# Kernel tuning notes

Hardware: AMD Instinct MI355X
Metric: run time of the kernel (lower is better)

The kernel has to match this reference:

```python
import jax, jax.numpy as jnp
import numpy as np

B, L, HID = 2, 4096, 2048
H, D = 16, HID // 16          # num_heads, head_dim = 128
C = 64                        # chunk_size
LOWR = 16                     # gate low-rank dim
GLN = 16.0                    # gate_logit_normalizer
EPS = 1e-5


def setup_inputs() -> dict:
    key = jax.random.key(0)
    ks = jax.random.split(key, 10)
    s = lambda fan_in: 1.0 / np.sqrt(fan_in)
    return {
        "x": jax.random.normal(ks[0], (B, L, HID), jnp.float32),
        "Wq": jax.random.normal(ks[1], (HID, HID), jnp.float32) * s(HID),
        "Wk": jax.random.normal(ks[2], (HID, HID), jnp.float32) * s(HID),
        "Wv": jax.random.normal(ks[3], (HID, HID), jnp.float32) * s(HID),
        "Wg1": jax.random.normal(ks[4], (HID, LOWR), jnp.float32) * s(HID),
        "Wg2": jax.random.normal(ks[5], (LOWR, HID), jnp.float32) * s(LOWR),
        "bg2": jax.random.normal(ks[6], (HID,), jnp.float32) * 0.1,
        "Wgate": jax.random.normal(ks[7], (HID, HID), jnp.float32) * s(HID),
        "norm_w": jnp.ones((D,), jnp.float32),
        "Wo": jax.random.normal(ks[8], (HID, HID), jnp.float32) * s(HID),
    }


def _gla_forward(x, Wq, Wk, Wv, Wg1, Wg2, bg2, Wgate, norm_w, Wo):
    Bx, Lx, _ = x.shape
    NC = Lx // C
    scale = D ** (-0.5)

    def heads(y):  # [B,L,HID] -> [B,H,L,D]
        return y.reshape(Bx, Lx, H, D).transpose(0, 2, 1, 3)

    q = heads(x @ Wq)
    k = heads(x @ Wk)
    v = heads(x @ Wv)
    gk = heads(jax.nn.log_sigmoid((x @ Wg1) @ Wg2 + bg2) / GLN)

    # chunked layout [NC,B,H,C,D]; cumulative log-gates within each chunk
    def chunked(y):
        return y.reshape(Bx, H, NC, C, D).transpose(2, 0, 1, 3, 4)

    qc, kc, vc = chunked(q), chunked(k), chunked(v)
    Gc = jnp.cumsum(chunked(gk), axis=3)

    tril = jnp.tril(jnp.ones((C, C), bool))
    S0 = jnp.zeros((Bx, H, D, D), jnp.float32)

    def step(S, inp):
        Q, K, V, G = inp                       # [B,H,C,D]
        Gbase = G[:, :, 0]                     # [B,H,D] cumsum at chunk start
        # inter-chunk: decayed query against carried state
        qg = Q * scale * jnp.exp(G)
        o_inter = jnp.einsum('bhld,bhdv->bhlv', qg, S)
        # intra-chunk causal attention with relative decay
        Qh = Q * jnp.exp(G - Gbase[:, :, None]) * scale
        Kh = K * jnp.exp(Gbase[:, :, None] - G)
        A = jnp.einsum('bhld,bhsd->bhls', Qh, Kh)
        A = jnp.where(tril, A, 0.0)
        o_intra = jnp.einsum('bhls,bhsv->bhlv', A, V)
        # state update
        glast = G[:, :, -1]                    # [B,H,D]
        Ks = K * jnp.exp(glast[:, :, None] - G)
        S_new = S * jnp.exp(glast)[..., None] + jnp.einsum('bhld,bhlv->bhdv', Ks, V)
        return S_new, o_inter + o_intra

    S_final, o_chunks = jax.lax.scan(step, S0, (qc, kc, vc, Gc))
    # [NC,B,H,C,D] -> [B,L,H,D]
    o = o_chunks.transpose(1, 3, 0, 2, 4).reshape(Bx, Lx, H, D)  # wrong order guard below
    o = o_chunks.transpose(1, 2, 0, 3, 4).reshape(Bx, H, Lx, D).transpose(0, 2, 1, 3)

    # RMSNorm over head_dim
    o = o * jax.lax.rsqrt(jnp.mean(o * o, axis=-1, keepdims=True) + EPS) * norm_w
    o = o.reshape(Bx, Lx, HID)

    g = x @ Wgate
    o = o * (g * jax.nn.sigmoid(g))            # swish output gate
    return o @ Wo, S_final


def reference(x, Wq, Wk, Wv, Wg1, Wg2, bg2, Wgate, norm_w, Wo):
    return _gla_forward(x, Wq, Wk, Wv, Wg1, Wg2, bg2, Wgate, norm_w, Wo)
```

## Files before the change

### kernel.cpp

```cpp
#include <hip/hip_runtime.h>
#include <math.h>

typedef __bf16 bf16;
typedef __attribute__((ext_vector_type(8))) __bf16 bf16x8;
typedef __attribute__((ext_vector_type(4))) __bf16 bf16x4;
typedef __attribute__((ext_vector_type(4))) float f32x4;

#define AS1 __attribute__((address_space(1)))
#define AS3 __attribute__((address_space(3)))

__device__ __forceinline__ void async16(const void* g, void* l) {
  __builtin_amdgcn_global_load_lds((AS1 void*)g, (AS3 void*)l, 16, 0, 0);
}

__device__ __forceinline__ f32x4 mfma16(bf16x8 a, bf16x8 b, f32x4 c) {
  return __builtin_amdgcn_mfma_f32_16x16x32_bf16(a, b, c, 0, 0, 0);
}

__device__ __forceinline__ float logsig(float z) {
  return fminf(z, 0.f) - __logf(1.f + __expf(-fabsf(z)));
}

static constexpr float SCALE = 0.088388347648318447f;


__global__ __launch_bounds__(256) void transpose_w(const float* __restrict__ W, bf16* __restrict__ Wt) {
  __shared__ float tl[64][65];
  int n0 = blockIdx.x * 64, k0 = blockIdx.y * 64;
  for (int e = threadIdx.x; e < 4096; e += 256) {
    int i = e >> 6, j = e & 63;
    tl[i][j] = W[(size_t)(k0 + i) * 2048 + n0 + j];
  }
  __syncthreads();
  for (int e = threadIdx.x; e < 4096; e += 256) {
    int i = e >> 6, j = e & 63;
    Wt[(size_t)(n0 + i) * 2048 + k0 + j] = (bf16)tl[j][i];
  }
}

__global__ __launch_bounds__(256) void cvt_x(const float* __restrict__ x, bf16* __restrict__ xb, int n) {
  for (size_t i = ((size_t)blockIdx.x * 256 + threadIdx.x) * 4; i < (size_t)n; i += (size_t)gridDim.x * 1024) {
    f32x4 v = *(const f32x4*)&x[i];
    bf16x4 o;
    #pragma unroll
    for (int j = 0; j < 4; ++j) o[j] = (bf16)v[j];
    *(bf16x4*)&xb[i] = o;
  }
}

__global__ __launch_bounds__(256) void cvt_wg1(const float* __restrict__ Wg1, bf16* __restrict__ Wg1t) {
  int k = blockIdx.x * 256 + threadIdx.x;
  #pragma unroll
  for (int j = 0; j < 16; ++j) Wg1t[j * 2048 + k] = (bf16)Wg1[(size_t)k * 16 + j];
}

__global__ __launch_bounds__(256) void xg_mfma(const bf16* __restrict__ xb, const bf16* __restrict__ Wg1t,
                                               float* __restrict__ xg) {
  int wave = threadIdx.x >> 6, lane = threadIdx.x & 63;
  int row0 = blockIdx.x * 64 + wave * 16;
  int rsel = lane & 15, klo = (lane >> 4) * 8;
  f32x4 acc = {0.f, 0.f, 0.f, 0.f};
  #pragma unroll 4
  for (int kt = 0; kt < 2048; kt += 32) {
    bf16x8 a = *(const bf16x8*)&xb[(size_t)(row0 + rsel) * 2048 + kt + klo];
    bf16x8 b = *(const bf16x8*)&Wg1t[rsel * 2048 + kt + klo];
    acc = mfma16(a, b, acc);
  }
  int col = lane & 15, r0 = (lane >> 4) * 4;
  #pragma unroll
  for (int r = 0; r < 4; ++r) xg[(size_t)(row0 + r0 + r) * 16 + col] = acc[r];
}


__device__ __forceinline__ int swzi(int r, int k0) { return r * 64 + ((((k0 >> 3) ^ r) & 7) << 3) + (k0 & 7); }

__device__ __forceinline__ void stage_half(const bf16* __restrict__ Gp, bf16* lds, int rbase, int kt, int h,
                                           int Kdim, int wave, int lane) {
  #pragma unroll
  for (int ii = 0; ii < 2; ++ii) {
    int i = 2 * h + ii;
    int row = (i * 8 + wave) * 8 + (lane >> 3);
    int gcol = (lane & 7) ^ ((lane >> 3) & 7);
    async16(&Gp[(size_t)(rbase + row) * Kdim + kt + gcol * 8], lds + (i * 8 + wave) * 512);
  }
}

template <int OUTF32>
__global__ __launch_bounds__(512, 2) void gemm256(const bf16* __restrict__ A, const bf16* __restrict__ Bt,
                                                  void* __restrict__ Cout, int Mdim, int Ndim, int Kdim) {
  __shared__ __align__(16) bf16 sA[2][256 * 64];
  __shared__ __align__(16) bf16 sB[2][256 * 64];

  int tid = threadIdx.x;
  int wave = tid >> 6, lane = tid & 63;
  int wr = wave >> 2, wc = wave & 3;
  int rsel = lane & 15, klo = (lane >> 4) * 8;

  int nwg = gridDim.x;
  int cpx = nwg >> 3;
  int bid = blockIdx.x;
  int swzb = (bid & 7) * cpx + (bid >> 3);
  int nbx = Ndim >> 8;
  int mt = (swzb / nbx) << 8, nt = (swzb % nbx) << 8;

  const int NT = Kdim >> 6;

  stage_half(A, &sA[0][0], mt, 0, 0, Kdim, wave, lane);
  stage_half(A, &sA[0][0], mt, 0, 1, Kdim, wave, lane);
  stage_half(Bt, &sB[0][0], nt, 0, 0, Kdim, wave, lane);
  stage_half(Bt, &sB[0][0], nt, 0, 1, Kdim, wave, lane);
  if (NT > 1) {
    stage_half(A, &sA[1][0], mt, 64, 0, Kdim, wave, lane);
    stage_half(A, &sA[1][0], mt, 64, 1, Kdim, wave, lane);
    stage_half(Bt, &sB[1][0], nt, 64, 0, Kdim, wave, lane);
    stage_half(Bt, &sB[1][0], nt, 64, 1, Kdim, wave, lane);
    asm volatile("s_waitcnt vmcnt(8)" ::: "memory");
  } else {
    asm volatile("s_waitcnt vmcnt(0)" ::: "memory");
  }
  __builtin_amdgcn_sched_barrier(0);
  __builtin_amdgcn_s_barrier();

  f32x4 z4 = {0.f, 0.f, 0.f, 0.f};
  f32x4 acc[8][4];
  #pragma unroll
  for (int i = 0; i < 8; ++i)
    #pragma unroll
    for (int j = 0; j < 4; ++j) acc[i][j] = z4;

  bf16x8 bfr[4][2];

  for (int t = 0; t < NT; ++t) {
    int b = t & 1;
    const bf16* __restrict__ cA = &sA[b][0];
    const bf16* __restrict__ cB = &sB[b][0];
    #pragma unroll
    for (int q = 0; q < 4; ++q) {
      bf16x8 af[2][2];
      if (q == 0) {
        #pragma unroll
        for (int nf = 0; nf < 4; ++nf)
          #pragma unroll
          for (int ks = 0; ks < 2; ++ks)
            bfr[nf][ks] = *(const bf16x8*)&cB[swzi(wc * 64 + nf * 16 + rsel, ks * 32 + klo)];
      }
      #pragma unroll
      for (int i = 0; i < 2; ++i)
        #pragma unroll
        for (int ks = 0; ks < 2; ++ks)
          af[i][ks] = *(const bf16x8*)&cA[swzi(wr * 128 + (2 * q + i) * 16 + rsel, ks * 32 + klo)];

      if (q < 2) {
        if (t >= 1 && t + 1 < NT) stage_half(A, &sA[(t + 1) & 1][0], mt, (t + 1) * 64, q, Kdim, wave, lane);
      } else {
        if (t + 2 < NT) stage_half(Bt, &sB[b][0], nt, (t + 2) * 64, q - 2, Kdim, wave, lane);
      }

      if (q == 3) {
        if (t + 2 < NT) {
          asm volatile("s_waitcnt vmcnt(4)" ::: "memory");
        } else if (t + 1 < NT) {
          asm volatile("s_waitcnt vmcnt(0)" ::: "memory");
        }
        __builtin_amdgcn_sched_barrier(0);
      }

      __builtin_amdgcn_s_barrier();
      asm volatile("s_waitcnt lgkmcnt(0)" ::: "memory");
      __builtin_amdgcn_sched_barrier(0);
      __builtin_amdgcn_s_setprio(1);
      #pragma unroll
      for (int i = 0; i < 2; ++i)
        #pragma unroll
        for (int nf = 0; nf < 4; ++nf)
          #pragma unroll
          for (int ks = 0; ks < 2; ++ks)
            acc[2 * q + i][nf] = mfma16(af[i][ks], bfr[nf][ks], acc[2 * q + i][nf]);
      __builtin_amdgcn_s_setprio(0);
      __builtin_amdgcn_s_barrier();
    }
  }

  int col0 = nt + wc * 64 + (lane & 15);
  int row0 = mt + wr * 128 + (lane >> 4) * 4;
  for (int mf = 0; mf < 8; ++mf)
    for (int nf = 0; nf < 4; ++nf)
      #pragma unroll
      for (int r = 0; r < 4; ++r) {
        size_t idx = (size_t)(row0 + mf * 16 + r) * Ndim + col0 + nf * 16;
        if constexpr (OUTF32 != 0)
          ((float*)Cout)[idx] = acc[mf][nf][r];
        else
          ((bf16*)Cout)[idx] = (bf16)acc[mf][nf][r];
      }
}


__global__ __launch_bounds__(256, 3) void gate_stage(bf16* __restrict__ qb, bf16* __restrict__ kb,
                                                     const float* __restrict__ xg, const float* __restrict__ Wg2,
                                                     const float* __restrict__ bg2, float* __restrict__ adec,
                                                     float* __restrict__ eg0) {
  __shared__ float G[64][132];
  __shared__ float xgs[1024];
  __shared__ float wg2s[2048];
  __shared__ float bg2s[128];
  int bid = blockIdx.x;
  int c = bid & 63, bh = bid >> 6, h = bh & 15;
  int l0row = (bh >> 4) * 4096 + c * 64;
  int tid = threadIdx.x;

  for (int e = tid; e < 1024; e += 256) xgs[e] = xg[(size_t)(l0row + (e >> 4)) * 16 + (e & 15)];
  for (int e = tid; e < 2048; e += 256) wg2s[e] = Wg2[(size_t)(e >> 7) * 2048 + h * 128 + (e & 127)];
  if (tid < 128) bg2s[tid] = bg2[h * 128 + tid];
  __syncthreads();

  {
    int d = tid & 127, half = tid >> 7;
    float w[16];
    #pragma unroll
    for (int j = 0; j < 16; ++j) w[j] = wg2s[j * 128 + d];
    float bz = bg2s[d];
    float run = 0.f;
    #pragma unroll 4
    for (int l = 0; l < 32; ++l) {
      int lr = half * 32 + l;
      float z = bz;
      #pragma unroll
      for (int j = 0; j < 16; ++j) z += xgs[lr * 16 + j] * w[j];
      run += logsig(z) * (1.0f / 16.0f);
      G[lr][d] = run;
    }
  }
  __syncthreads();
  {
    int d = tid & 127, half = tid >> 7;
    if (half) {
      float base = G[31][d];
      #pragma unroll 4
      for (int l = 32; l < 64; ++l) G[l][d] += base;
    }
  }
  __syncthreads();

  for (int it = 0; it < 4; ++it) {
    int l = (tid >> 4) + it * 16;
    int d0 = (tid & 15) * 8;
    size_t ro = (size_t)(l0row + l) * 2048 + h * 128 + d0;
    bf16x8 qv = *(const bf16x8*)&qb[ro];
    bf16x8 kv = *(const bf16x8*)&kb[ro];
    bf16x8 qo, ko;
    #pragma unroll
    for (int i = 0; i < 8; ++i) {
      int d = d0 + i;
      float Gl = G[l][d], Gb = G[0][d];
      qo[i] = (bf16)((float)qv[i] * SCALE * __expf(Gl - Gb));
      ko[i] = (bf16)((float)kv[i] * __expf(Gb - Gl));
    }
    *(bf16x8*)&qb[ro] = qo;
    *(bf16x8*)&kb[ro] = ko;
  }
  if (tid < 128) {
    float g63 = G[63][tid], g0 = G[0][tid];
    adec[(size_t)bid * 128 + tid] = __expf(g63);
    eg0[(size_t)bid * 128 + tid] = __expf(g0);
  }
}


__global__ __launch_bounds__(256, 4) void phaseA(const bf16* __restrict__ kh, const bf16* __restrict__ vb,
                                                 const float* __restrict__ adec, const float* __restrict__ eg0,
                                                 bf16* __restrict__ U) {
  __shared__ __align__(16) bf16 KhT[128][76];
  __shared__ __align__(16) bf16 VT[128][76];
  __shared__ float cscs[128];
  int bid = blockIdx.x;
  int c = bid & 63, bh = bid >> 6, h = bh & 15;
  int l0row = (bh >> 4) * 4096 + c * 64;
  int tid = threadIdx.x;
  if (tid < 128) cscs[tid] = adec[(size_t)bid * 128 + tid] / eg0[(size_t)bid * 128 + tid];

  for (int it = 0; it < 4; ++it) {
    int l = (tid >> 4) + it * 16;
    int d0 = (tid & 15) * 8;
    size_t ro = (size_t)(l0row + l) * 2048 + h * 128 + d0;
    bf16x8 kv = *(const bf16x8*)&kh[ro];
    bf16x8 vv = *(const bf16x8*)&vb[ro];
    #pragma unroll
    for (int i = 0; i < 8; ++i) {
      KhT[d0 + i][l] = kv[i];
      VT[d0 + i][l] = vv[i];
    }
  }
  __syncthreads();

  int wave = tid >> 6, lane = tid & 63;
  int rsel = lane & 15, klo = (lane >> 4) * 8;
  f32x4 z4 = {0.f, 0.f, 0.f, 0.f};
  f32x4 acc[2][8];
  for (int i = 0; i < 2; ++i)
    for (int j = 0; j < 8; ++j) acc[i][j] = z4;
  #pragma unroll
  for (int ks = 0; ks < 2; ++ks) {
    bf16x8 a0 = *(const bf16x8*)&VT[(wave * 2 + 0) * 16 + rsel][ks * 32 + klo];
    bf16x8 a1 = *(const bf16x8*)&VT[(wave * 2 + 1) * 16 + rsel][ks * 32 + klo];
    #pragma unroll
    for (int j = 0; j < 8; ++j) {
      bf16x8 bb = *(const bf16x8*)&KhT[j * 16 + rsel][ks * 32 + klo];
      acc[0][j] = mfma16(a0, bb, acc[0][j]);
      acc[1][j] = mfma16(a1, bb, acc[1][j]);
    }
  }
  size_t ub = (size_t)bid * 16384;
  for (int i = 0; i < 2; ++i)
    for (int j = 0; j < 8; ++j)
      #pragma unroll
      for (int r = 0; r < 4; ++r) {
        int vr = (wave * 2 + i) * 16 + (lane >> 4) * 4 + r;
        int d = j * 16 + (lane & 15);
        U[ub + (size_t)vr * 128 + d] = (bf16)(acc[i][j][r] * cscs[d]);
      }
}


__global__ __launch_bounds__(256) void phaseB(bf16* __restrict__ U, const float* __restrict__ adec,
                                              float* __restrict__ Sfin) {
  int bh = blockIdx.x >> 4, vg = blockIdx.x & 15;
  int t = threadIdx.x;
  int v = vg * 8 + (t >> 5);
  int d0 = (t & 31) * 4;
  float S[4] = {0.f, 0.f, 0.f, 0.f};
  size_t base = (size_t)bh * 64 * 16384 + (size_t)v * 128 + d0;
  size_t abase = (size_t)bh * 64 * 128 + d0;
  bf16x4 u = *(const bf16x4*)&U[base];
  f32x4 a = *(const f32x4*)&adec[abase];
  for (int c = 0; c < 64; ++c) {
    bf16x4 un = u;
    f32x4 an = a;
    if (c < 63) {
      un = *(const bf16x4*)&U[base + (size_t)(c + 1) * 16384];
      an = *(const f32x4*)&adec[abase + (size_t)(c + 1) * 128];
    }
    bf16x4 sv;
    #pragma unroll
    for (int i = 0; i < 4; ++i) sv[i] = (bf16)S[i];
    *(bf16x4*)&U[base + (size_t)c * 16384] = sv;
    #pragma unroll
    for (int i = 0; i < 4; ++i) S[i] = S[i] * a[i] + (float)u[i];
    u = un;
    a = an;
  }
  #pragma unroll
  for (int i = 0; i < 4; ++i) Sfin[((size_t)bh * 128 + d0 + i) * 128 + v] = S[i];
}


__global__ __launch_bounds__(256, 3) void phaseC(const bf16* __restrict__ qh, const bf16* __restrict__ kh,
                                                 const bf16* __restrict__ vb, const bf16* __restrict__ Sc,
                                                 const float* __restrict__ eg0, const bf16* __restrict__ gb,
                                                 const float* __restrict__ nw, bf16* __restrict__ ob) {
  __shared__ __align__(16) char lds[48384];
  bf16(*Qh)[136] = (bf16(*)[136])(lds);
  bf16(*VT)[76] = (bf16(*)[76])(lds + 17408);
  bf16(*A_lds)[76] = (bf16(*)[76])(lds + 36864);
  float* eG0s = (float*)(lds + 46592);
  float* red = (float*)(lds + 47104);
  float* rsq = (float*)(lds + 48128);
  float(*o_lds)[132] = (float(*)[132])(lds);

  int bid = blockIdx.x;
  int c = bid & 63, bh = bid >> 6, h = bh & 15;
  int l0row = (bh >> 4) * 4096 + c * 64;
  int tid = threadIdx.x;

  for (int it = 0; it < 4; ++it) {
    int e = tid + it * 256;
    int l = e >> 4, d0 = (e & 15) * 8;
    *(bf16x8*)&Qh[l][d0] = *(const bf16x8*)&qh[(size_t)(l0row + l) * 2048 + h * 128 + d0];
  }
  for (int it = 0; it < 4; ++it) {
    int l = (tid >> 4) + it * 16;
    int d0 = (tid & 15) * 8;
    bf16x8 vv = *(const bf16x8*)&vb[(size_t)(l0row + l) * 2048 + h * 128 + d0];
    #pragma unroll
    for (int i = 0; i < 8; ++i) VT[d0 + i][l] = vv[i];
  }
  if (tid < 128) eG0s[tid] = eg0[(size_t)bid * 128 + tid];
  __syncthreads();

  int wave = tid >> 6, lane = tid & 63;
  int rsel = lane & 15, klo = (lane >> 4) * 8;
  f32x4 z4 = {0.f, 0.f, 0.f, 0.f};

  bf16x8 bbk[4];
  #pragma unroll
  for (int ks = 0; ks < 4; ++ks)
    bbk[ks] = *(const bf16x8*)&kh[(size_t)(l0row + wave * 16 + rsel) * 2048 + h * 128 + ks * 32 + klo];
  bf16x8 scr[4][2];
  #pragma unroll
  for (int ks = 0; ks < 4; ++ks)
    #pragma unroll
    for (int j = 0; j < 2; ++j)
      scr[ks][j] =
          *(const bf16x8*)&Sc[(size_t)bid * 16384 + (size_t)((wave * 2 + j) * 16 + rsel) * 128 + ks * 32 + klo];

  f32x4 accA[4];
  for (int i = 0; i < 4; ++i) accA[i] = z4;
  #pragma unroll
  for (int ks = 0; ks < 4; ++ks)
    #pragma unroll
    for (int mf = 0; mf < 4; ++mf) {
      bf16x8 aa = *(const bf16x8*)&Qh[mf * 16 + rsel][ks * 32 + klo];
      accA[mf] = mfma16(aa, bbk[ks], accA[mf]);
    }
  #pragma unroll
  for (int mf = 0; mf < 4; ++mf)
    #pragma unroll
    for (int r = 0; r < 4; ++r) {
      int lrow = mf * 16 + (lane >> 4) * 4 + r;
      int scol = wave * 16 + (lane & 15);
      A_lds[lrow][scol] = (bf16)(scol <= lrow ? accA[mf][r] : 0.0f);
    }

  bf16x8 bs[4][2];
  #pragma unroll
  for (int ks = 0; ks < 4; ++ks)
    #pragma unroll
    for (int j = 0; j < 2; ++j)
      #pragma unroll
      for (int i = 0; i < 8; ++i) bs[ks][j][i] = (bf16)((float)scr[ks][j][i] * eG0s[ks * 32 + klo + i]);

  f32x4 accO[4][2];
  for (int i = 0; i < 4; ++i)
    for (int j = 0; j < 2; ++j) accO[i][j] = z4;
  #pragma unroll
  for (int ks = 0; ks < 4; ++ks)
    #pragma unroll
    for (int mf = 0; mf < 4; ++mf) {
      bf16x8 aa = *(const bf16x8*)&Qh[mf * 16 + rsel][ks * 32 + klo];
      accO[mf][0] = mfma16(aa, bs[ks][0], accO[mf][0]);
      accO[mf][1] = mfma16(aa, bs[ks][1], accO[mf][1]);
    }
  __syncthreads();

  #pragma unroll
  for (int ks = 0; ks < 2; ++ks) {
    bf16x8 b0 = *(const bf16x8*)&VT[(wave * 2 + 0) * 16 + rsel][ks * 32 + klo];
    bf16x8 b1 = *(const bf16x8*)&VT[(wave * 2 + 1) * 16 + rsel][ks * 32 + klo];
    #pragma unroll
    for (int mf = 0; mf < 4; ++mf) {
      bf16x8 aa = *(const bf16x8*)&A_lds[mf * 16 + rsel][ks * 32 + klo];
      accO[mf][0] = mfma16(aa, b0, accO[mf][0]);
      accO[mf][1] = mfma16(aa, b1, accO[mf][1]);
    }
  }
  __syncthreads();

  #pragma unroll
  for (int mf = 0; mf < 4; ++mf)
    #pragma unroll
    for (int j = 0; j < 2; ++j)
      #pragma unroll
      for (int r = 0; r < 4; ++r)
        o_lds[mf * 16 + (lane >> 4) * 4 + r][(wave * 2 + j) * 16 + (lane & 15)] = accO[mf][j][r];
  __syncthreads();

  {
    int row = tid >> 2, part = tid & 3;
    float ss = 0.f;
    #pragma unroll
    for (int i = 0; i < 32; ++i) {
      float xv = o_lds[row][part * 32 + i];
      ss += xv * xv;
    }
    red[row * 4 + part] = ss;
  }
  __syncthreads();
  if (tid < 64) {
    float s = red[tid * 4] + red[tid * 4 + 1] + red[tid * 4 + 2] + red[tid * 4 + 3];
    rsq[tid] = rsqrtf(s * (1.0f / 128.0f) + 1e-5f);
  }
  __syncthreads();
  for (int e = tid; e < 8192; e += 256) {
    int l = e >> 7, d = e & 127;
    float ov = o_lds[l][d] * rsq[l] * nw[d];
    float gf = (float)gb[(size_t)(l0row + l) * 2048 + h * 128 + d];
    float sil = gf / (1.0f + __expf(-gf));
    ob[(size_t)(l0row + l) * 2048 + h * 128 + d] = (bf16)(ov * sil);
  }
}


extern "C" void kernel_launch(void* const* d_in, const int* in_sizes, int n_in, void* d_out, int out_size,
                              void* d_ws, size_t ws_size, hipStream_t stream) {
  const float* x = (const float*)d_in[0];
  const float* Wq = (const float*)d_in[1];
  const float* Wk = (const float*)d_in[2];
  const float* Wv = (const float*)d_in[3];
  const float* Wg1 = (const float*)d_in[4];
  const float* Wg2 = (const float*)d_in[5];
  const float* bg2 = (const float*)d_in[6];
  const float* Wgate = (const float*)d_in[7];
  const float* nw = (const float*)d_in[8];
  const float* Wo = (const float*)d_in[9];
  float* out1 = (float*)d_out;
  float* out2 = out1 + (size_t)8192 * 2048;

  const size_t WT_B = (size_t)2048 * 2048 * 2;
  const size_t XG_B = (size_t)8192 * 16 * 4;
  const size_t WG1_B = (size_t)16 * 2048 * 2;
  const size_t TOK_B = (size_t)8192 * 2048 * 2;
  const size_t VEC_B = (size_t)2048 * 128 * 4;
  const size_t U_B = (size_t)32 * 64 * 16384 * 2;

  char* ws = (char*)d_ws;
  bf16* Wt = (bf16*)ws;
  float* xgf = (float*)(ws + WT_B);
  bf16* Wg1t = (bf16*)(ws + WT_B + XG_B);
  bf16* qb = (bf16*)(ws + WT_B + XG_B + WG1_B);
  bf16* kbuf = (bf16*)(ws + WT_B + XG_B + WG1_B + TOK_B);
  bf16* vbuf = (bf16*)(ws + WT_B + XG_B + WG1_B + 2 * TOK_B);
  bf16* gbuf = (bf16*)(ws + WT_B + XG_B + WG1_B + 3 * TOK_B);
  float* adecf = (float*)(ws + WT_B + XG_B + WG1_B + 4 * TOK_B);
  float* eg0f = (float*)(ws + WT_B + XG_B + WG1_B + 4 * TOK_B + VEC_B);
  bf16* Ub = (bf16*)(ws + WT_B + XG_B + WG1_B + 4 * TOK_B + 2 * VEC_B);
  bf16* xb = Ub;
  const size_t NEED = WT_B + XG_B + WG1_B + 4 * TOK_B + 2 * VEC_B + U_B;
  if (ws_size < NEED) return;

  dim3 tg(32, 32);

  cvt_x<<<4096, 256, 0, stream>>>(x, xb, 8192 * 2048);
  cvt_wg1<<<8, 256, 0, stream>>>(Wg1, Wg1t);
  xg_mfma<<<128, 256, 0, stream>>>(xb, Wg1t, xgf);

  transpose_w<<<tg, 256, 0, stream>>>(Wq, Wt);
  gemm256<0><<<256, 512, 0, stream>>>(xb, Wt, qb, 8192, 2048, 2048);
  transpose_w<<<tg, 256, 0, stream>>>(Wk, Wt);
  gemm256<0><<<256, 512, 0, stream>>>(xb, Wt, kbuf, 8192, 2048, 2048);
  transpose_w<<<tg, 256, 0, stream>>>(Wv, Wt);
  gemm256<0><<<256, 512, 0, stream>>>(xb, Wt, vbuf, 8192, 2048, 2048);
  transpose_w<<<tg, 256, 0, stream>>>(Wgate, Wt);
  gemm256<0><<<256, 512, 0, stream>>>(xb, Wt, gbuf, 8192, 2048, 2048);

  gate_stage<<<2048, 256, 0, stream>>>(qb, kbuf, xgf, Wg2, bg2, adecf, eg0f);
  phaseA<<<2048, 256, 0, stream>>>(kbuf, vbuf, adecf, eg0f, Ub);
  phaseB<<<512, 256, 0, stream>>>(Ub, adecf, out2);
  phaseC<<<2048, 256, 0, stream>>>(qb, kbuf, vbuf, Ub, eg0f, gbuf, nw, qb);

  transpose_w<<<tg, 256, 0, stream>>>(Wo, Wt);
  gemm256<1><<<256, 512, 0, stream>>>(qb, Wt, out1, 8192, 2048, 2048);
}
```

Measured before the change: 601.8 us.

## Restructure GEMM main loop with register double-buffered fragments and one barrier per tile

Rewrites the 256x256 bf16 GEMM inner loop. LDS fragment reads now ping-pong between two register sets so the next A/B fragments load while the current MFMA phase runs. The per-quarter s_barrier/lgkmcnt pairs become a single barrier per K-tile, and the first fragments of the next tile are read ahead of the last MFMA phase. In exchange, global prefetch drops from two tiles ahead to one with a full vmcnt(0) wait each tile, which may expose memory latency. LDS reads issued just before the barrier are not explicitly waited on, leaving a subtle buffer-reuse ordering risk.

```diff
diff --git a/kernel.cpp b/kernel.cpp
--- a/kernel.cpp
+++ b/kernel.cpp
@@ -85,6 +85,20 @@
   }
 }
 
+__device__ __forceinline__ void mfma_phase(f32x4 (&acc)[8][4], int row0, const bf16x8 (&AF)[2][2],
+                                           const bf16x8 (&B0)[4], const bf16x8 (&B1)[4]) {
+  __builtin_amdgcn_sched_barrier(0);
+  __builtin_amdgcn_s_setprio(1);
+  #pragma unroll
+  for (int ks = 0; ks < 2; ++ks)
+    #pragma unroll
+    for (int i = 0; i < 2; ++i)
+      #pragma unroll
+      for (int nf = 0; nf < 4; ++nf)
+        acc[row0 + i][nf] = mfma16(AF[i][ks], ks ? B1[nf] : B0[nf], acc[row0 + i][nf]);
+  __builtin_amdgcn_s_setprio(0);
+}
+
 template <int OUTF32>
 __global__ __launch_bounds__(512, 2) void gemm256(const bf16* __restrict__ A, const bf16* __restrict__ Bt,
                                                   void* __restrict__ Cout, int Mdim, int Ndim, int Kdim) {
@@ -105,21 +119,27 @@
 
   const int NT = Kdim >> 6;
 
+  auto rdA = [&](bf16x8 (&dst)[2][2], const bf16* base, int m0) {
+    #pragma unroll
+    for (int i = 0; i < 2; ++i)
+      #pragma unroll
+      for (int ks = 0; ks < 2; ++ks)
+        dst[i][ks] = *(const bf16x8*)&base[swzi(wr * 128 + (m0 + i) * 16 + rsel, ks * 32 + klo)];
+  };
+  auto rdB = [&](bf16x8 (&dst)[4], const bf16* base, int ks) {
+    #pragma unroll
+    for (int nf = 0; nf < 4; ++nf)
+      dst[nf] = *(const bf16x8*)&base[swzi(wc * 64 + nf * 16 + rsel, ks * 32 + klo)];
+  };
+
   stage_half(A, &sA[0][0], mt, 0, 0, Kdim, wave, lane);
   stage_half(A, &sA[0][0], mt, 0, 1, Kdim, wave, lane);
   stage_half(Bt, &sB[0][0], nt, 0, 0, Kdim, wave, lane);
   stage_half(Bt, &sB[0][0], nt, 0, 1, Kdim, wave, lane);
-  if (NT > 1) {
-    stage_half(A, &sA[1][0], mt, 64, 0, Kdim, wave, lane);
-    stage_half(A, &sA[1][0], mt, 64, 1, Kdim, wave, lane);
-    stage_half(Bt, &sB[1][0], nt, 64, 0, Kdim, wave, lane);
-    stage_half(Bt, &sB[1][0], nt, 64, 1, Kdim, wave, lane);
-    asm volatile("s_waitcnt vmcnt(8)" ::: "memory");
-  } else {
-    asm volatile("s_waitcnt vmcnt(0)" ::: "memory");
-  }
+  asm volatile("s_waitcnt vmcnt(0)" ::: "memory");
   __builtin_amdgcn_sched_barrier(0);
   __builtin_amdgcn_s_barrier();
+  __builtin_amdgcn_sched_barrier(0);
 
   f32x4 z4 = {0.f, 0.f, 0.f, 0.f};
   f32x4 acc[8][4];
@@ -128,57 +148,58 @@
     #pragma unroll
     for (int j = 0; j < 4; ++j) acc[i][j] = z4;
 
-  bf16x8 bfr[4][2];
+  bf16x8 aP[2][2], aQ[2][2], b0[4], b1[4];
+  rdB(b0, &sB[0][0], 0);
+  rdA(aP, &sA[0][0], 0);
 
   for (int t = 0; t < NT; ++t) {
-    int b = t & 1;
-    const bf16* __restrict__ cA = &sA[b][0];
-    const bf16* __restrict__ cB = &sB[b][0];
-    #pragma unroll
-    for (int q = 0; q < 4; ++q) {
-      bf16x8 af[2][2];
-      if (q == 0) {
-        #pragma unroll
-        for (int nf = 0; nf < 4; ++nf)
-          #pragma unroll
-          for (int ks = 0; ks < 2; ++ks)
-            bfr[nf][ks] = *(const bf16x8*)&cB[swzi(wc * 64 + nf * 16 + rsel, ks * 32 + klo)];
-      }
-      #pragma unroll
-      for (int i = 0; i < 2; ++i)
-        #pragma unroll
-        for (int ks = 0; ks < 2; ++ks)
-          af[i][ks] = *(const bf16x8*)&cA[swzi(wr * 128 + (2 * q + i) * 16 + rsel, ks * 32 + klo)];
-
-      if (q < 2) {
-        if (t >= 1 && t + 1 < NT) stage_half(A, &sA[(t + 1) & 1][0], mt, (t + 1) * 64, q, Kdim, wave, lane);
-      } else {
-        if (t + 2 < NT) stage_half(Bt, &sB[b][0], nt, (t + 2) * 64, q - 2, Kdim, wave, lane);
-      }
-
-      if (q == 3) {
-        if (t + 2 < NT) {
-          asm volatile("s_waitcnt vmcnt(4)" ::: "memory");
-        } else if (t + 1 < NT) {
-          asm volatile("s_waitcnt vmcnt(0)" ::: "memory");
-        }
-        __builtin_amdgcn_sched_barrier(0);
-      }
-
+    const bf16* cA = &sA[t & 1][0];
+    const bf16* cB = &sB[t & 1][0];
+    bf16* nAp = &sA[(t & 1) ^ 1][0];
+    bf16* nBp = &sB[(t & 1) ^ 1][0];
+    bool more = (t + 1) < NT;
+
+    if (more) {
+      stage_half(A, nAp, mt, (t + 1) * 64, 0, Kdim, wave, lane);
+      stage_half(A, nAp, mt, (t + 1) * 64, 1, Kdim, wave, lane);
+    }
+    rdB(b1, cB, 1);
+    rdA(aQ, cA, 2);
+    mfma_phase(acc, 0, aP, b0, b1);
+
+    if (more) {
+      stage_half(Bt, nBp, nt, (t + 1) * 64, 0, Kdim, wave, lane);
+      stage_half(Bt, nBp, nt, (t + 1) * 64, 1, Kdim, wave, lane);
+    }
+    rdA(aP, cA, 4);
+    mfma_phase(acc, 2, aQ, b0, b1);
+
+    rdA(aQ, cA, 6);
+    mfma_phase(acc, 4, aP, b0, b1);
+    if (more) {
+      asm volatile("s_waitcnt vmcnt(0)" ::: "memory");
+      __builtin_amdgcn_sched_barrier(0);
       __builtin_amdgcn_s_barrier();
-      asm volatile("s_waitcnt lgkmcnt(0)" ::: "memory");
       __builtin_amdgcn_sched_barrier(0);
-      __builtin_amdgcn_s_setprio(1);
-      #pragma unroll
-      for (int i = 0; i < 2; ++i)
-        #pragma unroll
-        for (int nf = 0; nf < 4; ++nf)
-          #pragma unroll
-          for (int ks = 0; ks < 2; ++ks)
-            acc[2 * q + i][nf] = mfma16(af[i][ks], bfr[nf][ks], acc[2 * q + i][nf]);
-      __builtin_amdgcn_s_setprio(0);
-      __builtin_amdgcn_s_barrier();
-    }
+    }
+
+    __builtin_amdgcn_s_setprio(1);
+    #pragma unroll
+    for (int i = 0; i < 2; ++i)
+      #pragma unroll
+      for (int nf = 0; nf < 4; ++nf) acc[6 + i][nf] = mfma16(aQ[i][0], b0[nf], acc[6 + i][nf]);
+    __builtin_amdgcn_s_setprio(0);
+    if (more) {
+      rdB(b0, nBp, 0);
+      rdA(aP, nAp, 0);
+    }
+    __builtin_amdgcn_sched_barrier(0);
+    __builtin_amdgcn_s_setprio(1);
+    #pragma unroll
+    for (int i = 0; i < 2; ++i)
+      #pragma unroll
+      for (int nf = 0; nf < 4; ++nf) acc[6 + i][nf] = mfma16(aQ[i][1], b1[nf], acc[6 + i][nf]);
+    __builtin_amdgcn_s_setprio(0);
   }
 
   int col0 = nt + wc * 64 + (lane & 15);
```

Result: faster. 565.9 us (-6.0%).

## Fuse Q/K/V/gate projections into one GEMM and deepen LDS pipeline

Applied to the files above, without the earlier changes.

The four projection GEMMs become a single 8192x8192x2048 launch over concatenated transposed weights. The output is scattered into the separate q/k/v/g buffers through a group stride. The GEMM main loop now stages K-tiles of 32 into a 4-deep LDS ring buffer with register double-buffering of fragments, so prefetch overlaps MFMA work. The intent is to cut launch overhead and tail effects and to hide global load latency better, at the cost of more complex wait accounting and reuse of the U workspace region for the weights.

```diff
diff --git a/kernel.cpp b/kernel.cpp
--- a/kernel.cpp
+++ b/kernel.cpp
@@ -72,24 +72,28 @@
 }
 
 
-__device__ __forceinline__ int swzi(int r, int k0) { return r * 64 + ((((k0 >> 3) ^ r) & 7) << 3) + (k0 & 7); }
-
-__device__ __forceinline__ void stage_half(const bf16* __restrict__ Gp, bf16* lds, int rbase, int kt, int h,
-                                           int Kdim, int wave, int lane) {
-  #pragma unroll
-  for (int ii = 0; ii < 2; ++ii) {
-    int i = 2 * h + ii;
-    int row = (i * 8 + wave) * 8 + (lane >> 3);
-    int gcol = (lane & 7) ^ ((lane >> 3) & 7);
-    async16(&Gp[(size_t)(rbase + row) * Kdim + kt + gcol * 8], lds + (i * 8 + wave) * 512);
+__device__ __forceinline__ int swz32(int r, int k0) {
+  int g = ((k0 >> 3) ^ (r & 3) ^ ((r >> 2) & 3)) & 3;
+  return r * 32 + g * 8 + (k0 & 7);
+}
+
+__device__ __forceinline__ void stage32(const bf16* __restrict__ Gp, bf16* lds, int rbase, int kt, int Kdim,
+                                        int tid) {
+  #pragma unroll
+  for (int i = 0; i < 2; ++i) {
+    int slot = i * 512 + tid;
+    int row = slot >> 2, gr = slot & 3;
+    int gsrc = (gr ^ (row & 3) ^ ((row >> 2) & 3)) & 3;
+    async16(&Gp[(size_t)(rbase + row) * Kdim + kt + gsrc * 8], lds + slot * 8);
   }
 }
 
 template <int OUTF32>
 __global__ __launch_bounds__(512, 2) void gemm256(const bf16* __restrict__ A, const bf16* __restrict__ Bt,
-                                                  void* __restrict__ Cout, int Mdim, int Ndim, int Kdim) {
-  __shared__ __align__(16) bf16 sA[2][256 * 64];
-  __shared__ __align__(16) bf16 sB[2][256 * 64];
+                                                  void* __restrict__ Cout, int Mdim, int Ndim, int Kdim,
+                                                  size_t groupStride) {
+  __shared__ __align__(16) bf16 sA[4][256 * 32];
+  __shared__ __align__(16) bf16 sB[4][256 * 32];
 
   int tid = threadIdx.x;
   int wave = tid >> 6, lane = tid & 63;
@@ -103,23 +107,29 @@
   int nbx = Ndim >> 8;
   int mt = (swzb / nbx) << 8, nt = (swzb % nbx) << 8;
 
-  const int NT = Kdim >> 6;
-
-  stage_half(A, &sA[0][0], mt, 0, 0, Kdim, wave, lane);
-  stage_half(A, &sA[0][0], mt, 0, 1, Kdim, wave, lane);
-  stage_half(Bt, &sB[0][0], nt, 0, 0, Kdim, wave, lane);
-  stage_half(Bt, &sB[0][0], nt, 0, 1, Kdim, wave, lane);
-  if (NT > 1) {
-    stage_half(A, &sA[1][0], mt, 64, 0, Kdim, wave, lane);
-    stage_half(A, &sA[1][0], mt, 64, 1, Kdim, wave, lane);
-    stage_half(Bt, &sB[1][0], nt, 64, 0, Kdim, wave, lane);
-    stage_half(Bt, &sB[1][0], nt, 64, 1, Kdim, wave, lane);
-    asm volatile("s_waitcnt vmcnt(8)" ::: "memory");
-  } else {
-    asm volatile("s_waitcnt vmcnt(0)" ::: "memory");
-  }
+  const int NT = Kdim >> 5;
+
+  auto rdA4 = [&](bf16x8 (&dst)[4], const bf16* base, int m0) {
+    #pragma unroll
+    for (int i = 0; i < 4; ++i)
+      dst[i] = *(const bf16x8*)&base[swz32(wr * 128 + (m0 + i) * 16 + rsel, klo)];
+  };
+  auto rdB4 = [&](bf16x8 (&dst)[4], const bf16* base) {
+    #pragma unroll
+    for (int nf = 0; nf < 4; ++nf)
+      dst[nf] = *(const bf16x8*)&base[swz32(wc * 64 + nf * 16 + rsel, klo)];
+  };
+
+  stage32(A, &sA[0][0], mt, 0, Kdim, tid);
+  stage32(Bt, &sB[0][0], nt, 0, Kdim, tid);
+  stage32(A, &sA[1][0], mt, 32, Kdim, tid);
+  stage32(Bt, &sB[1][0], nt, 32, Kdim, tid);
+  stage32(A, &sA[2][0], mt, 64, Kdim, tid);
+  stage32(Bt, &sB[2][0], nt, 64, Kdim, tid);
+  asm volatile("s_waitcnt vmcnt(8)" ::: "memory");
   __builtin_amdgcn_sched_barrier(0);
   __builtin_amdgcn_s_barrier();
+  __builtin_amdgcn_sched_barrier(0);
 
   f32x4 z4 = {0.f, 0.f, 0.f, 0.f};
   f32x4 acc[8][4];
@@ -128,66 +138,64 @@
     #pragma unroll
     for (int j = 0; j < 4; ++j) acc[i][j] = z4;
 
-  bf16x8 bfr[4][2];
+  bf16x8 aP[4], aQ[4], bC[4], aPn[4], bN[4];
+  rdB4(bC, &sB[0][0]);
+  rdA4(aP, &sA[0][0], 0);
 
   for (int t = 0; t < NT; ++t) {
-    int b = t & 1;
-    const bf16* __restrict__ cA = &sA[b][0];
-    const bf16* __restrict__ cB = &sB[b][0];
-    #pragma unroll
-    for (int q = 0; q < 4; ++q) {
-      bf16x8 af[2][2];
-      if (q == 0) {
-        #pragma unroll
-        for (int nf = 0; nf < 4; ++nf)
-          #pragma unroll
-          for (int ks = 0; ks < 2; ++ks)
-            bfr[nf][ks] = *(const bf16x8*)&cB[swzi(wc * 64 + nf * 16 + rsel, ks * 32 + klo)];
-      }
-      #pragma unroll
-      for (int i = 0; i < 2; ++i)
-        #pragma unroll
-        for (int ks = 0; ks < 2; ++ks)
-          af[i][ks] = *(const bf16x8*)&cA[swzi(wr * 128 + (2 * q + i) * 16 + rsel, ks * 32 + klo)];
-
-      if (q < 2) {
-        if (t >= 1 && t + 1 < NT) stage_half(A, &sA[(t + 1) & 1][0], mt, (t + 1) * 64, q, Kdim, wave, lane);
-      } else {
-        if (t + 2 < NT) stage_half(Bt, &sB[b][0], nt, (t + 2) * 64, q - 2, Kdim, wave, lane);
-      }
-
-      if (q == 3) {
-        if (t + 2 < NT) {
-          asm volatile("s_waitcnt vmcnt(4)" ::: "memory");
-        } else if (t + 1 < NT) {
-          asm volatile("s_waitcnt vmcnt(0)" ::: "memory");
-        }
-        __builtin_amdgcn_sched_barrier(0);
-      }
-
-      __builtin_amdgcn_s_barrier();
-      asm volatile("s_waitcnt lgkmcnt(0)" ::: "memory");
-      __builtin_amdgcn_sched_barrier(0);
-      __builtin_amdgcn_s_setprio(1);
-      #pragma unroll
-      for (int i = 0; i < 2; ++i)
-        #pragma unroll
-        for (int nf = 0; nf < 4; ++nf)
-          #pragma unroll
-          for (int ks = 0; ks < 2; ++ks)
-            acc[2 * q + i][nf] = mfma16(af[i][ks], bfr[nf][ks], acc[2 * q + i][nf]);
-      __builtin_amdgcn_s_setprio(0);
-      __builtin_amdgcn_s_barrier();
-    }
-  }
-
-  int col0 = nt + wc * 64 + (lane & 15);
+    const bf16* cA = &sA[t & 3][0];
+    const bf16* cB = &sB[t & 3][0];
+
+    if (t + 3 < NT) {
+      stage32(A, &sA[(t + 3) & 3][0], mt, (t + 3) * 32, Kdim, tid);
+      stage32(Bt, &sB[(t + 3) & 3][0], nt, (t + 3) * 32, Kdim, tid);
+    }
+    rdA4(aQ, cA, 4);
+    __builtin_amdgcn_sched_barrier(0);
+    __builtin_amdgcn_s_setprio(1);
+    #pragma unroll
+    for (int i = 0; i < 4; ++i)
+      #pragma unroll
+      for (int nf = 0; nf < 4; ++nf) acc[i][nf] = mfma16(aP[i], bC[nf], acc[i][nf]);
+    __builtin_amdgcn_s_setprio(0);
+
+    if (t + 3 < NT) {
+      asm volatile("s_waitcnt vmcnt(8)" ::: "memory");
+    } else if (t + 2 < NT) {
+      asm volatile("s_waitcnt vmcnt(4)" ::: "memory");
+    } else if (t + 1 < NT) {
+      asm volatile("s_waitcnt vmcnt(0)" ::: "memory");
+    }
+    __builtin_amdgcn_sched_barrier(0);
+    __builtin_amdgcn_s_barrier();
+    __builtin_amdgcn_sched_barrier(0);
+
+    if (t + 1 < NT) {
+      rdB4(bN, &sB[(t + 1) & 3][0]);
+      rdA4(aPn, &sA[(t + 1) & 3][0], 0);
+    }
+    __builtin_amdgcn_sched_barrier(0);
+    __builtin_amdgcn_s_setprio(1);
+    #pragma unroll
+    for (int i = 0; i < 4; ++i)
+      #pragma unroll
+      for (int nf = 0; nf < 4; ++nf) acc[4 + i][nf] = mfma16(aQ[i], bC[nf], acc[4 + i][nf]);
+    __builtin_amdgcn_s_setprio(0);
+    #pragma unroll
+    for (int i = 0; i < 4; ++i) {
+      aP[i] = aPn[i];
+      bC[i] = bN[i];
+    }
+  }
+
+  int colg = nt + wc * 64 + (lane & 15);
+  int grp = colg >> 11, colw = colg & 2047;
   int row0 = mt + wr * 128 + (lane >> 4) * 4;
   for (int mf = 0; mf < 8; ++mf)
     for (int nf = 0; nf < 4; ++nf)
       #pragma unroll
       for (int r = 0; r < 4; ++r) {
-        size_t idx = (size_t)(row0 + mf * 16 + r) * Ndim + col0 + nf * 16;
+        size_t idx = (size_t)grp * groupStride + (size_t)(row0 + mf * 16 + r) * 2048 + colw + nf * 16;
         if constexpr (OUTF32 != 0)
           ((float*)Cout)[idx] = acc[mf][nf][r];
         else
@@ -505,7 +513,6 @@
   float* out1 = (float*)d_out;
   float* out2 = out1 + (size_t)8192 * 2048;
 
-  const size_t WT_B = (size_t)2048 * 2048 * 2;
   const size_t XG_B = (size_t)8192 * 16 * 4;
   const size_t WG1_B = (size_t)16 * 2048 * 2;
   const size_t TOK_B = (size_t)8192 * 2048 * 2;
@@ -513,18 +520,20 @@
   const size_t U_B = (size_t)32 * 64 * 16384 * 2;
 
   char* ws = (char*)d_ws;
-  bf16* Wt = (bf16*)ws;
-  float* xgf = (float*)(ws + WT_B);
-  bf16* Wg1t = (bf16*)(ws + WT_B + XG_B);
-  bf16* qb = (bf16*)(ws + WT_B + XG_B + WG1_B);
-  bf16* kbuf = (bf16*)(ws + WT_B + XG_B + WG1_B + TOK_B);
-  bf16* vbuf = (bf16*)(ws + WT_B + XG_B + WG1_B + 2 * TOK_B);
-  bf16* gbuf = (bf16*)(ws + WT_B + XG_B + WG1_B + 3 * TOK_B);
-  float* adecf = (float*)(ws + WT_B + XG_B + WG1_B + 4 * TOK_B);
-  float* eg0f = (float*)(ws + WT_B + XG_B + WG1_B + 4 * TOK_B + VEC_B);
-  bf16* Ub = (bf16*)(ws + WT_B + XG_B + WG1_B + 4 * TOK_B + 2 * VEC_B);
-  bf16* xb = Ub;
-  const size_t NEED = WT_B + XG_B + WG1_B + 4 * TOK_B + 2 * VEC_B + U_B;
+  float* xgf = (float*)ws;
+  bf16* Wg1t = (bf16*)(ws + XG_B);
+  bf16* qb = (bf16*)(ws + XG_B + WG1_B);
+  bf16* kbuf = (bf16*)(ws + XG_B + WG1_B + TOK_B);
+  bf16* vbuf = (bf16*)(ws + XG_B + WG1_B + 2 * TOK_B);
+  bf16* gbuf = (bf16*)(ws + XG_B + WG1_B + 3 * TOK_B);
+  float* adecf = (float*)(ws + XG_B + WG1_B + 4 * TOK_B);
+  float* eg0f = (float*)(ws + XG_B + WG1_B + 4 * TOK_B + VEC_B);
+  char* Ureg = ws + XG_B + WG1_B + 4 * TOK_B + 2 * VEC_B;
+  bf16* Ub = (bf16*)Ureg;
+  bf16* xb = (bf16*)Ureg;
+  bf16* Wt4 = (bf16*)(Ureg + TOK_B);
+  bf16* WtO = (bf16*)Ureg;
+  const size_t NEED = XG_B + WG1_B + 4 * TOK_B + 2 * VEC_B + U_B;
   if (ws_size < NEED) return;
 
   dim3 tg(32, 32);
@@ -533,20 +542,18 @@
   cvt_wg1<<<8, 256, 0, stream>>>(Wg1, Wg1t);
   xg_mfma<<<128, 256, 0, stream>>>(xb, Wg1t, xgf);
 
-  transpose_w<<<tg, 256, 0, stream>>>(Wq, Wt);
-  gemm256<0><<<256, 512, 0, stream>>>(xb, Wt, qb, 8192, 2048, 2048);
-  transpose_w<<<tg, 256, 0, stream>>>(Wk, Wt);
-  gemm256<0><<<256, 512, 0, stream>>>(xb, Wt, kbuf, 8192, 2048, 2048);
-  transpose_w<<<tg, 256, 0, stream>>>(Wv, Wt);
-  gemm256<0><<<256, 512, 0, stream>>>(xb, Wt, vbuf, 8192, 2048, 2048);
-  transpose_w<<<tg, 256, 0, stream>>>(Wgate, Wt);
-  gemm256<0><<<256, 512, 0, stream>>>(xb, Wt, gbuf, 8192, 2048, 2048);
+  transpose_w<<<tg, 256, 0, stream>>>(Wq, Wt4);
+  transpose_w<<<tg, 256, 0, stream>>>(Wk, Wt4 + (size_t)2048 * 2048);
+  transpose_w<<<tg, 256, 0, stream>>>(Wv, Wt4 + (size_t)2 * 2048 * 2048);
+  transpose_w<<<tg, 256, 0, stream>>>(Wgate, Wt4 + (size_t)3 * 2048 * 2048);
+
+  gemm256<0><<<1024, 512, 0, stream>>>(xb, Wt4, qb, 8192, 8192, 2048, (size_t)8192 * 2048);
 
   gate_stage<<<2048, 256, 0, stream>>>(qb, kbuf, xgf, Wg2, bg2, adecf, eg0f);
   phaseA<<<2048, 256, 0, stream>>>(kbuf, vbuf, adecf, eg0f, Ub);
   phaseB<<<512, 256, 0, stream>>>(Ub, adecf, out2);
   phaseC<<<2048, 256, 0, stream>>>(qb, kbuf, vbuf, Ub, eg0f, gbuf, nw, qb);
 
-  transpose_w<<<tg, 256, 0, stream>>>(Wo, Wt);
-  gemm256<1><<<256, 512, 0, stream>>>(qb, Wt, out1, 8192, 2048, 2048);
-}
+  transpose_w<<<tg, 256, 0, stream>>>(Wo, WtO);
+  gemm256<1><<<256, 512, 0, stream>>>(qb, WtO, out1, 8192, 2048, 2048, (size_t)8192 * 2048);
+}
```

Measured after the change: 649.6 us. +7.9%, slower.
